# Kernel tuning notes

Hardware: AMD Instinct MI355X
Metric: run time of the kernel (lower is better)

The kernel has to match this reference:

```python
import jax, jax.numpy as jnp
import numpy as np
import math

D_MODEL = 1024
NUM_HEADS = 16
N_GROUP = 4
HEAD_DIM = D_MODEL // NUM_HEADS  # 64
KV_DIM = N_GROUP * HEAD_DIM      # 256
BS, SEQ = 2, 2048


def setup_inputs() -> dict:
    key = jax.random.key(0)
    ks = jax.random.split(key, 7)
    s = 0.02
    return {
        "h": jax.random.normal(ks[0], (BS, SEQ, D_MODEL), dtype=jnp.float32),
        "wq_w": jax.random.normal(ks[1], (D_MODEL, D_MODEL), dtype=jnp.float32) * s,
        "wq_b": jnp.zeros((D_MODEL,), dtype=jnp.float32),
        "wk_w": jax.random.normal(ks[2], (KV_DIM, D_MODEL), dtype=jnp.float32) * s,
        "wk_b": jnp.zeros((KV_DIM,), dtype=jnp.float32),
        "wv_w": jax.random.normal(ks[3], (KV_DIM, D_MODEL), dtype=jnp.float32) * s,
        "wv_b": jnp.zeros((KV_DIM,), dtype=jnp.float32),
    }


def reference(h, wq_w, wq_b, wk_w, wk_b, wv_w, wv_b):
    bs, seq, _ = h.shape
    rep = NUM_HEADS // N_GROUP  # heads per KV group

    # Linear projections (torch Linear: x @ W.T + b)
    q = h @ wq_w.T + wq_b                     # [bs, seq, d_model]
    k = h @ wk_w.T + wk_b                     # [bs, seq, kv_dim]
    v = h @ wv_w.T + wv_b                     # [bs, seq, kv_dim]

    q = q.reshape(bs, seq, NUM_HEADS, HEAD_DIM).transpose(0, 2, 1, 3)  # [b,H,s,d]
    k = k.reshape(bs, seq, N_GROUP, HEAD_DIM)                          # [b,s,G,d]
    v = v.reshape(bs, seq, N_GROUP, HEAD_DIM)
    # torch .repeat(1,1,1,rep).view(...,num_heads,head_dim) maps head h -> group h//rep,
    # identical to repeating each group `rep` times consecutively along the head axis.
    k = jnp.repeat(k, rep, axis=2).transpose(0, 2, 1, 3)               # [b,H,s,d]
    v = jnp.repeat(v, rep, axis=2).transpose(0, 2, 1, 3)               # [b,H,s,d]

    scores = jnp.einsum("bhqd,bhkd->bhqk", q, k) / math.sqrt(HEAD_DIM)
    attn = jax.nn.softmax(scores, axis=-1)
    out = jnp.einsum("bhqk,bhkd->bhqd", attn, v)                       # [b,H,s,d]
    out = out.transpose(0, 2, 1, 3).reshape(bs, seq, NUM_HEADS * HEAD_DIM)
    return out
```

## Files before the change

kernel.cpp:

```cpp
#include <hip/hip_runtime.h>

typedef _Float16 f16;
typedef _Float16 f16x8 __attribute__((ext_vector_type(8)));
typedef _Float16 f16x4 __attribute__((ext_vector_type(4)));
typedef float f32x4 __attribute__((ext_vector_type(4)));

#define MFMA16(a, b, c) __builtin_amdgcn_mfma_f32_16x16x32_f16((a), (b), (c), 0, 0, 0)
#define GLDS16(g, l)                                                        \
    __builtin_amdgcn_global_load_lds(                                       \
        (const __attribute__((address_space(1))) void*)(g),                 \
        (__attribute__((address_space(3))) void*)(l), 16, 0, 0)

#define SEQ 2048
#define DMODEL 1024
#define NH 16
#define NG 4

__global__ __launch_bounds__(256) void cvt_f16(const float* __restrict__ src,
                                               f16* __restrict__ dst, int n4) {
    int i = blockIdx.x * 256 + threadIdx.x;
    if (i < n4) {
        const float4 v = ((const float4*)src)[i];
        f16x4 p;
        p[0] = (f16)v.x; p[1] = (f16)v.y; p[2] = (f16)v.z; p[3] = (f16)v.w;
        ((f16x4*)dst)[i] = p;
    }
}

__global__ __launch_bounds__(256) void qkv_gemm(const f16* __restrict__ hA,
                                                const f16* __restrict__ wq,
                                                const f16* __restrict__ wk,
                                                const f16* __restrict__ wv,
                                                const float* __restrict__ bq,
                                                const float* __restrict__ bk,
                                                const float* __restrict__ bv,
                                                f16* __restrict__ Qb,
                                                f16* __restrict__ Kb,
                                                f16* __restrict__ Vtb,
                                                float qscale) {
    __shared__ __align__(16) f16 As[128 * 32];
    __shared__ __align__(16) f16 Bs[128 * 32];

    const int tid  = threadIdx.x;
    const int lane = tid & 63;
    const int l15  = lane & 15;
    const int l4   = lane >> 4;
    const int wave = tid >> 6;
    const int wm   = (wave >> 1) * 64;
    const int wn   = (wave & 1) * 64;
    const int bx   = blockIdx.x;
    const int m0   = blockIdx.y * 128;

    const f16* Bmat; const float* bias; f16* C; int N, n0; float osc; int vmode;
    if (bx < 8)       { Bmat = wq; bias = bq; C = Qb;  N = 1024; n0 = bx * 128;        osc = qscale; vmode = 0; }
    else if (bx < 10) { Bmat = wk; bias = bk; C = Kb;  N = 256;  n0 = (bx - 8) * 128;  osc = 1.0f;   vmode = 0; }
    else              { Bmat = wv; bias = bv; C = Vtb; N = 256;  n0 = (bx - 10) * 128; osc = 1.0f;   vmode = 1; }

    const int rowA = tid >> 2;
    const int colA = (tid & 3) * 8;
    const f16* Ag = hA   + (size_t)(m0 + rowA) * DMODEL + colA;
    const f16* Bg = Bmat + (size_t)(n0 + rowA) * DMODEL + colA;
    f16* AsW0 = As + wave * 512;
    f16* AsW1 = As + 2048 + wave * 512;
    f16* BsW0 = Bs + wave * 512;
    f16* BsW1 = Bs + 2048 + wave * 512;

    f32x4 acc[4][4];
#pragma unroll
    for (int i = 0; i < 4; i++)
#pragma unroll
        for (int j = 0; j < 4; j++) acc[i][j] = (f32x4)0.0f;

    for (int k0 = 0; k0 < DMODEL; k0 += 32) {
        GLDS16(Ag + k0,         AsW0);
        GLDS16(Ag + 65536 + k0, AsW1);
        GLDS16(Bg + k0,         BsW0);
        GLDS16(Bg + 65536 + k0, BsW1);
        __syncthreads();

        f16x8 af[4], bf[4];
#pragma unroll
        for (int i = 0; i < 4; i++)
            af[i] = *(const f16x8*)&As[(wm + i * 16 + l15) * 32 + l4 * 8];
#pragma unroll
        for (int j = 0; j < 4; j++)
            bf[j] = *(const f16x8*)&Bs[(wn + j * 16 + l15) * 32 + l4 * 8];
#pragma unroll
        for (int i = 0; i < 4; i++)
#pragma unroll
            for (int j = 0; j < 4; j++)
                acc[i][j] = MFMA16(af[i], bf[j], acc[i][j]);
        __syncthreads();
    }

#pragma unroll
    for (int i = 0; i < 4; i++) {
        const int mbase = m0 + wm + i * 16 + l4 * 4;
#pragma unroll
        for (int j = 0; j < 4; j++) {
            const int n  = n0 + wn + j * 16 + l15;
            const float bv = bias[n];
            if (vmode == 0) {
#pragma unroll
                for (int r = 0; r < 4; r++)
                    C[(size_t)(mbase + r) * N + n] = (f16)((acc[i][j][r] + bv) * osc);
            } else {
                f16x4 p;
#pragma unroll
                for (int r = 0; r < 4; r++)
                    p[r] = (f16)((acc[i][j][r] + bv) * osc);
                const int bb = mbase >> 11;
                const int s  = mbase & 2047;
                *(f16x4*)&C[((size_t)(bb * 256 + n)) * SEQ + s] = p;
            }
        }
    }
}

__global__ __launch_bounds__(256, 4) void attn_kernel(const f16* __restrict__ Q,
                                                      const f16* __restrict__ Kt,
                                                      const f16* __restrict__ Vt,
                                                      float* __restrict__ out) {
    __shared__ __align__(16) f16 Ks[64 * 72];
    __shared__ __align__(16) f16 Vs[64 * 72];
    __shared__ __align__(16) f16 Ps[64 * 72];

    const int tid  = threadIdx.x;
    const int lane = tid & 63;
    const int l15  = lane & 15;
    const int l4   = lane >> 4;
    const int wave = tid >> 6;
    const int b    = blockIdx.z;
    const int hh   = blockIdx.y;
    const int g    = hh >> 2;
    const int q0   = blockIdx.x * 64;
    const int qw   = wave * 16;

    f16x8 qf[2];
#pragma unroll
    for (int kt = 0; kt < 2; kt++)
        qf[kt] = *(const f16x8*)&Q[((size_t)(b * SEQ + q0 + qw + l15)) * DMODEL + hh * 64 + kt * 32 + l4 * 8];

    f32x4 oacc[4];
    float lsum[4];
#pragma unroll
    for (int dt = 0; dt < 4; dt++) oacc[dt] = (f32x4)0.0f;
#pragma unroll
    for (int r = 0; r < 4; r++) lsum[r] = 0.0f;

    const int srow = tid >> 2;
    const int sc8  = (tid & 3) * 8;
    const f16* Kg = Kt + (size_t)(b * SEQ + srow) * 256 + g * 64 + sc8;
    const f16* Vg = Vt + (size_t)(b * 256 + g * 64 + srow) * SEQ + sc8;

    for (int kb = 0; kb < SEQ; kb += 64) {
        *(f16x8*)&Ks[srow * 72 + sc8]      = *(const f16x8*)(Kg + (size_t)kb * 256);
        *(f16x8*)&Ks[srow * 72 + 32 + sc8] = *(const f16x8*)(Kg + (size_t)kb * 256 + 32);
        *(f16x8*)&Vs[srow * 72 + sc8]      = *(const f16x8*)(Vg + kb);
        *(f16x8*)&Vs[srow * 72 + 32 + sc8] = *(const f16x8*)(Vg + kb + 32);
        __syncthreads();

        f32x4 sacc[4];
#pragma unroll
        for (int jt = 0; jt < 4; jt++) sacc[jt] = (f32x4)0.0f;
#pragma unroll
        for (int jt = 0; jt < 4; jt++) {
            const f16x8 kf0 = *(const f16x8*)&Ks[(jt * 16 + l15) * 72 + l4 * 8];
            const f16x8 kf1 = *(const f16x8*)&Ks[(jt * 16 + l15) * 72 + 32 + l4 * 8];
            sacc[jt] = MFMA16(qf[0], kf0, sacc[jt]);
            sacc[jt] = MFMA16(qf[1], kf1, sacc[jt]);
        }

#pragma unroll
        for (int jt = 0; jt < 4; jt++)
#pragma unroll
            for (int r = 0; r < 4; r++) {
                const float p = exp2f(fminf(sacc[jt][r], 14.0f));
                lsum[r] += p;
                Ps[(qw + l4 * 4 + r) * 72 + jt * 16 + l15] = (f16)p;
            }

#pragma unroll
        for (int kt = 0; kt < 2; kt++) {
            const f16x8 pf = *(const f16x8*)&Ps[(qw + l15) * 72 + kt * 32 + l4 * 8];
#pragma unroll
            for (int dt = 0; dt < 4; dt++) {
                const f16x8 vf = *(const f16x8*)&Vs[(dt * 16 + l15) * 72 + kt * 32 + l4 * 8];
                oacc[dt] = MFMA16(pf, vf, oacc[dt]);
            }
        }
        __syncthreads();
    }

#pragma unroll
    for (int r = 0; r < 4; r++) {
        float l = lsum[r];
        l += __shfl_xor(l, 1);
        l += __shfl_xor(l, 2);
        l += __shfl_xor(l, 4);
        l += __shfl_xor(l, 8);
        const float inv = 1.0f / l;
        const int q = q0 + qw + l4 * 4 + r;
        float* op = out + ((size_t)(b * SEQ + q)) * DMODEL + hh * 64;
#pragma unroll
        for (int dt = 0; dt < 4; dt++)
            op[dt * 16 + l15] = oacc[dt][r] * inv;
    }
}

extern "C" void kernel_launch(void* const* d_in, const int* in_sizes, int n_in,
                              void* d_out, int out_size, void* d_ws, size_t ws_size,
                              hipStream_t stream) {
    const float* h    = (const float*)d_in[0];
    const float* wq_w = (const float*)d_in[1];
    const float* wq_b = (const float*)d_in[2];
    const float* wk_w = (const float*)d_in[3];
    const float* wk_b = (const float*)d_in[4];
    const float* wv_w = (const float*)d_in[5];
    const float* wv_b = (const float*)d_in[6];
    float* out = (float*)d_out;

    char* ws = (char*)d_ws;
    f16* hb  = (f16*)(ws + 0);
    f16* wqb = (f16*)(ws + 8388608);
    f16* wkb = (f16*)(ws + 10485760);
    f16* wvb = (f16*)(ws + 11010048);
    f16* Qb  = (f16*)(ws + 11534336);
    f16* Kb  = (f16*)(ws + 19922944);
    f16* Vtb = (f16*)(ws + 22020096);

    cvt_f16<<<4096, 256, 0, stream>>>(h, hb, 1048576);
    cvt_f16<<<1024, 256, 0, stream>>>(wq_w, wqb, 262144);
    cvt_f16<<<256,  256, 0, stream>>>(wk_w, wkb, 65536);
    cvt_f16<<<256,  256, 0, stream>>>(wv_w, wvb, 65536);

    const float qscale = 0.125f * 1.4426950408889634f;
    qkv_gemm<<<dim3(12, 32), 256, 0, stream>>>(hb, wqb, wkb, wvb, wq_b, wk_b, wv_b,
                                               Qb, Kb, Vtb, qscale);

    attn_kernel<<<dim3(32, 16, 2), 256, 0, stream>>>(Qb, Kb, Vtb, out);
}
```

Baseline: 191.0 us.

## Fuse conversions, narrow GEMM tiles, process two heads per attention block

The four fp32-to-fp16 conversion launches become one kernel. The QKV GEMM N-tile shrinks from 128 to 64, doubling the grid to 768 blocks for better CU fill. The attention kernel now handles two heads of the same KV group per block, so each staged K/V tile is reused twice and K/V global loads are halved. LDS padding changes to 76. The cost is more registers and LDS per attention block (occupancy hint lowered to 2) and only 512 attention blocks.

Result: no change. 191.6 us (+0.3%).

```diff
diff --git a/kernel.cpp b/kernel.cpp
--- a/kernel.cpp
+++ b/kernel.cpp
@@ -15,31 +15,39 @@
 #define DMODEL 1024
 #define NH 16
 #define NG 4
-
-__global__ __launch_bounds__(256) void cvt_f16(const float* __restrict__ src,
-                                               f16* __restrict__ dst, int n4) {
-    int i = blockIdx.x * 256 + threadIdx.x;
-    if (i < n4) {
-        const float4 v = ((const float4*)src)[i];
-        f16x4 p;
-        p[0] = (f16)v.x; p[1] = (f16)v.y; p[2] = (f16)v.z; p[3] = (f16)v.w;
-        ((f16x4*)dst)[i] = p;
-    }
-}
-
-__global__ __launch_bounds__(256) void qkv_gemm(const f16* __restrict__ hA,
-                                                const f16* __restrict__ wq,
-                                                const f16* __restrict__ wk,
-                                                const f16* __restrict__ wv,
-                                                const float* __restrict__ bq,
-                                                const float* __restrict__ bk,
-                                                const float* __restrict__ bv,
-                                                f16* __restrict__ Qb,
-                                                f16* __restrict__ Kb,
-                                                f16* __restrict__ Vtb,
-                                                float qscale) {
+#define PAD 76
+
+__global__ __launch_bounds__(256) void cvt_all(const float* __restrict__ h,
+                                               const float* __restrict__ wq,
+                                               const float* __restrict__ wk,
+                                               const float* __restrict__ wv,
+                                               f16* __restrict__ hb, f16* __restrict__ wqb,
+                                               f16* __restrict__ wkb, f16* __restrict__ wvb) {
+    const int i = blockIdx.x * 256 + threadIdx.x;
+    const float* s; f16* d; int off;
+    if (i < 1048576)      { s = h;  d = hb;  off = i; }
+    else if (i < 1310720) { s = wq; d = wqb; off = i - 1048576; }
+    else if (i < 1376256) { s = wk; d = wkb; off = i - 1310720; }
+    else                  { s = wv; d = wvb; off = i - 1376256; }
+    const float4 v = ((const float4*)s)[off];
+    f16x4 p;
+    p[0] = (f16)v.x; p[1] = (f16)v.y; p[2] = (f16)v.z; p[3] = (f16)v.w;
+    ((f16x4*)d)[off] = p;
+}
+
+__global__ __launch_bounds__(256, 3) void qkv_gemm(const f16* __restrict__ hA,
+                                                   const f16* __restrict__ wq,
+                                                   const f16* __restrict__ wk,
+                                                   const f16* __restrict__ wv,
+                                                   const float* __restrict__ bq,
+                                                   const float* __restrict__ bk,
+                                                   const float* __restrict__ bv,
+                                                   f16* __restrict__ Qb,
+                                                   f16* __restrict__ Kb,
+                                                   f16* __restrict__ Vtb,
+                                                   float qscale) {
     __shared__ __align__(16) f16 As[128 * 32];
-    __shared__ __align__(16) f16 Bs[128 * 32];
+    __shared__ __align__(16) f16 Bs[64 * 32];
 
     const int tid  = threadIdx.x;
     const int lane = tid & 63;
@@ -47,48 +55,46 @@
     const int l4   = lane >> 4;
     const int wave = tid >> 6;
     const int wm   = (wave >> 1) * 64;
-    const int wn   = (wave & 1) * 64;
+    const int wn   = (wave & 1) * 32;
     const int bx   = blockIdx.x;
     const int m0   = blockIdx.y * 128;
 
-    const f16* Bmat; const float* bias; f16* C; int N, n0; float osc; int vmode;
-    if (bx < 8)       { Bmat = wq; bias = bq; C = Qb;  N = 1024; n0 = bx * 128;        osc = qscale; vmode = 0; }
-    else if (bx < 10) { Bmat = wk; bias = bk; C = Kb;  N = 256;  n0 = (bx - 8) * 128;  osc = 1.0f;   vmode = 0; }
-    else              { Bmat = wv; bias = bv; C = Vtb; N = 256;  n0 = (bx - 10) * 128; osc = 1.0f;   vmode = 1; }
-
-    const int rowA = tid >> 2;
-    const int colA = (tid & 3) * 8;
-    const f16* Ag = hA   + (size_t)(m0 + rowA) * DMODEL + colA;
-    const f16* Bg = Bmat + (size_t)(n0 + rowA) * DMODEL + colA;
+    const f16* W; const float* bias; f16* C; int N, n0; float osc; int vmode;
+    if (bx < 16)      { W = wq; bias = bq; C = Qb;  N = 1024; n0 = bx * 64;        osc = qscale; vmode = 0; }
+    else if (bx < 20) { W = wk; bias = bk; C = Kb;  N = 256;  n0 = (bx - 16) * 64; osc = 1.0f;   vmode = 0; }
+    else              { W = wv; bias = bv; C = Vtb; N = 256;  n0 = (bx - 20) * 64; osc = 1.0f;   vmode = 1; }
+
+    const int rowT = tid >> 2;
+    const int colT = (tid & 3) * 8;
+    const f16* Ag = hA + (size_t)(m0 + rowT) * DMODEL + colT;
+    const f16* Bg = W  + (size_t)(n0 + rowT) * DMODEL + colT;
     f16* AsW0 = As + wave * 512;
     f16* AsW1 = As + 2048 + wave * 512;
-    f16* BsW0 = Bs + wave * 512;
-    f16* BsW1 = Bs + 2048 + wave * 512;
-
-    f32x4 acc[4][4];
+    f16* BsW  = Bs + wave * 512;
+
+    f32x4 acc[4][2];
 #pragma unroll
     for (int i = 0; i < 4; i++)
 #pragma unroll
-        for (int j = 0; j < 4; j++) acc[i][j] = (f32x4)0.0f;
+        for (int j = 0; j < 2; j++) acc[i][j] = (f32x4)0.0f;
 
     for (int k0 = 0; k0 < DMODEL; k0 += 32) {
         GLDS16(Ag + k0,         AsW0);
         GLDS16(Ag + 65536 + k0, AsW1);
-        GLDS16(Bg + k0,         BsW0);
-        GLDS16(Bg + 65536 + k0, BsW1);
-        __syncthreads();
-
-        f16x8 af[4], bf[4];
+        GLDS16(Bg + k0,         BsW);
+        __syncthreads();
+
+        f16x8 af[4], bf[2];
 #pragma unroll
         for (int i = 0; i < 4; i++)
             af[i] = *(const f16x8*)&As[(wm + i * 16 + l15) * 32 + l4 * 8];
 #pragma unroll
-        for (int j = 0; j < 4; j++)
+        for (int j = 0; j < 2; j++)
             bf[j] = *(const f16x8*)&Bs[(wn + j * 16 + l15) * 32 + l4 * 8];
 #pragma unroll
         for (int i = 0; i < 4; i++)
 #pragma unroll
-            for (int j = 0; j < 4; j++)
+            for (int j = 0; j < 2; j++)
                 acc[i][j] = MFMA16(af[i], bf[j], acc[i][j]);
         __syncthreads();
     }
@@ -97,7 +103,7 @@
     for (int i = 0; i < 4; i++) {
         const int mbase = m0 + wm + i * 16 + l4 * 4;
 #pragma unroll
-        for (int j = 0; j < 4; j++) {
+        for (int j = 0; j < 2; j++) {
             const int n  = n0 + wn + j * 16 + l15;
             const float bv = bias[n];
             if (vmode == 0) {
@@ -117,13 +123,13 @@
     }
 }
 
-__global__ __launch_bounds__(256, 4) void attn_kernel(const f16* __restrict__ Q,
+__global__ __launch_bounds__(256, 2) void attn_kernel(const f16* __restrict__ Q,
                                                       const f16* __restrict__ Kt,
                                                       const f16* __restrict__ Vt,
                                                       float* __restrict__ out) {
-    __shared__ __align__(16) f16 Ks[64 * 72];
-    __shared__ __align__(16) f16 Vs[64 * 72];
-    __shared__ __align__(16) f16 Ps[64 * 72];
+    __shared__ __align__(16) f16 Ks[64 * PAD];
+    __shared__ __align__(16) f16 Vs[64 * PAD];
+    __shared__ __align__(16) f16 Ps[128 * PAD];
 
     const int tid  = threadIdx.x;
     const int lane = tid & 63;
@@ -131,22 +137,29 @@
     const int l4   = lane >> 4;
     const int wave = tid >> 6;
     const int b    = blockIdx.z;
-    const int hh   = blockIdx.y;
-    const int g    = hh >> 2;
+    const int hp   = blockIdx.y;
+    const int g    = hp >> 1;
     const int q0   = blockIdx.x * 64;
     const int qw   = wave * 16;
 
-    f16x8 qf[2];
-#pragma unroll
-    for (int kt = 0; kt < 2; kt++)
-        qf[kt] = *(const f16x8*)&Q[((size_t)(b * SEQ + q0 + qw + l15)) * DMODEL + hh * 64 + kt * 32 + l4 * 8];
-
-    f32x4 oacc[4];
-    float lsum[4];
-#pragma unroll
-    for (int dt = 0; dt < 4; dt++) oacc[dt] = (f32x4)0.0f;
-#pragma unroll
-    for (int r = 0; r < 4; r++) lsum[r] = 0.0f;
+    f16x8 qf[2][2];
+#pragma unroll
+    for (int h = 0; h < 2; h++)
+#pragma unroll
+        for (int kt = 0; kt < 2; kt++)
+            qf[h][kt] = *(const f16x8*)&Q[((size_t)(b * SEQ + q0 + qw + l15)) * DMODEL
+                                          + (hp * 2 + h) * 64 + kt * 32 + l4 * 8];
+
+    f32x4 oacc[2][4];
+    float lsum[2][4];
+#pragma unroll
+    for (int h = 0; h < 2; h++)
+#pragma unroll
+        for (int dt = 0; dt < 4; dt++) oacc[h][dt] = (f32x4)0.0f;
+#pragma unroll
+    for (int h = 0; h < 2; h++)
+#pragma unroll
+        for (int r = 0; r < 4; r++) lsum[h][r] = 0.0f;
 
     const int srow = tid >> 2;
     const int sc8  = (tid & 3) * 8;
@@ -154,58 +167,69 @@
     const f16* Vg = Vt + (size_t)(b * 256 + g * 64 + srow) * SEQ + sc8;
 
     for (int kb = 0; kb < SEQ; kb += 64) {
-        *(f16x8*)&Ks[srow * 72 + sc8]      = *(const f16x8*)(Kg + (size_t)kb * 256);
-        *(f16x8*)&Ks[srow * 72 + 32 + sc8] = *(const f16x8*)(Kg + (size_t)kb * 256 + 32);
-        *(f16x8*)&Vs[srow * 72 + sc8]      = *(const f16x8*)(Vg + kb);
-        *(f16x8*)&Vs[srow * 72 + 32 + sc8] = *(const f16x8*)(Vg + kb + 32);
-        __syncthreads();
-
-        f32x4 sacc[4];
-#pragma unroll
-        for (int jt = 0; jt < 4; jt++) sacc[jt] = (f32x4)0.0f;
+        *(f16x8*)&Ks[srow * PAD + sc8]      = *(const f16x8*)(Kg + (size_t)kb * 256);
+        *(f16x8*)&Ks[srow * PAD + 32 + sc8] = *(const f16x8*)(Kg + (size_t)kb * 256 + 32);
+        *(f16x8*)&Vs[srow * PAD + sc8]      = *(const f16x8*)(Vg + kb);
+        *(f16x8*)&Vs[srow * PAD + 32 + sc8] = *(const f16x8*)(Vg + kb + 32);
+        __syncthreads();
+
+        f32x4 sacc[2][4];
+#pragma unroll
+        for (int h = 0; h < 2; h++)
+#pragma unroll
+            for (int jt = 0; jt < 4; jt++) sacc[h][jt] = (f32x4)0.0f;
 #pragma unroll
         for (int jt = 0; jt < 4; jt++) {
-            const f16x8 kf0 = *(const f16x8*)&Ks[(jt * 16 + l15) * 72 + l4 * 8];
-            const f16x8 kf1 = *(const f16x8*)&Ks[(jt * 16 + l15) * 72 + 32 + l4 * 8];
-            sacc[jt] = MFMA16(qf[0], kf0, sacc[jt]);
-            sacc[jt] = MFMA16(qf[1], kf1, sacc[jt]);
-        }
-
-#pragma unroll
-        for (int jt = 0; jt < 4; jt++)
-#pragma unroll
-            for (int r = 0; r < 4; r++) {
-                const float p = exp2f(fminf(sacc[jt][r], 14.0f));
-                lsum[r] += p;
-                Ps[(qw + l4 * 4 + r) * 72 + jt * 16 + l15] = (f16)p;
+            const f16x8 kf0 = *(const f16x8*)&Ks[(jt * 16 + l15) * PAD + l4 * 8];
+            const f16x8 kf1 = *(const f16x8*)&Ks[(jt * 16 + l15) * PAD + 32 + l4 * 8];
+#pragma unroll
+            for (int h = 0; h < 2; h++) {
+                sacc[h][jt] = MFMA16(qf[h][0], kf0, sacc[h][jt]);
+                sacc[h][jt] = MFMA16(qf[h][1], kf1, sacc[h][jt]);
             }
+        }
+
+#pragma unroll
+        for (int h = 0; h < 2; h++)
+#pragma unroll
+            for (int jt = 0; jt < 4; jt++)
+#pragma unroll
+                for (int r = 0; r < 4; r++) {
+                    const float p = exp2f(fminf(sacc[h][jt][r], 14.0f));
+                    lsum[h][r] += p;
+                    Ps[(h * 64 + qw + l4 * 4 + r) * PAD + jt * 16 + l15] = (f16)p;
+                }
 
 #pragma unroll
         for (int kt = 0; kt < 2; kt++) {
-            const f16x8 pf = *(const f16x8*)&Ps[(qw + l15) * 72 + kt * 32 + l4 * 8];
+            const f16x8 pf0 = *(const f16x8*)&Ps[(qw + l15) * PAD + kt * 32 + l4 * 8];
+            const f16x8 pf1 = *(const f16x8*)&Ps[(64 + qw + l15) * PAD + kt * 32 + l4 * 8];
 #pragma unroll
             for (int dt = 0; dt < 4; dt++) {
-                const f16x8 vf = *(const f16x8*)&Vs[(dt * 16 + l15) * 72 + kt * 32 + l4 * 8];
-                oacc[dt] = MFMA16(pf, vf, oacc[dt]);
+                const f16x8 vf = *(const f16x8*)&Vs[(dt * 16 + l15) * PAD + kt * 32 + l4 * 8];
+                oacc[0][dt] = MFMA16(pf0, vf, oacc[0][dt]);
+                oacc[1][dt] = MFMA16(pf1, vf, oacc[1][dt]);
             }
         }
         __syncthreads();
     }
 
 #pragma unroll
-    for (int r = 0; r < 4; r++) {
-        float l = lsum[r];
-        l += __shfl_xor(l, 1);
-        l += __shfl_xor(l, 2);
-        l += __shfl_xor(l, 4);
-        l += __shfl_xor(l, 8);
-        const float inv = 1.0f / l;
-        const int q = q0 + qw + l4 * 4 + r;
-        float* op = out + ((size_t)(b * SEQ + q)) * DMODEL + hh * 64;
-#pragma unroll
-        for (int dt = 0; dt < 4; dt++)
-            op[dt * 16 + l15] = oacc[dt][r] * inv;
-    }
+    for (int h = 0; h < 2; h++)
+#pragma unroll
+        for (int r = 0; r < 4; r++) {
+            float l = lsum[h][r];
+            l += __shfl_xor(l, 1);
+            l += __shfl_xor(l, 2);
+            l += __shfl_xor(l, 4);
+            l += __shfl_xor(l, 8);
+            const float inv = 1.0f / l;
+            const int q = q0 + qw + l4 * 4 + r;
+            float* op = out + ((size_t)(b * SEQ + q)) * DMODEL + (hp * 2 + h) * 64;
+#pragma unroll
+            for (int dt = 0; dt < 4; dt++)
+                op[dt * 16 + l15] = oacc[h][dt][r] * inv;
+        }
 }
 
 extern "C" void kernel_launch(void* const* d_in, const int* in_sizes, int n_in,
@@ -229,14 +253,11 @@
     f16* Kb  = (f16*)(ws + 19922944);
     f16* Vtb = (f16*)(ws + 22020096);
 
-    cvt_f16<<<4096, 256, 0, stream>>>(h, hb, 1048576);
-    cvt_f16<<<1024, 256, 0, stream>>>(wq_w, wqb, 262144);
-    cvt_f16<<<256,  256, 0, stream>>>(wk_w, wkb, 65536);
-    cvt_f16<<<256,  256, 0, stream>>>(wv_w, wvb, 65536);
+    cvt_all<<<5632, 256, 0, stream>>>(h, wq_w, wk_w, wv_w, hb, wqb, wkb, wvb);
 
     const float qscale = 0.125f * 1.4426950408889634f;
-    qkv_gemm<<<dim3(12, 32), 256, 0, stream>>>(hb, wqb, wkb, wvb, wq_b, wk_b, wv_b,
+    qkv_gemm<<<dim3(24, 32), 256, 0, stream>>>(hb, wqb, wkb, wvb, wq_b, wk_b, wv_b,
                                                Qb, Kb, Vtb, qscale);
 
-    attn_kernel<<<dim3(32, 16, 2), 256, 0, stream>>>(Qb, Kb, Vtb, out);
-}
+    attn_kernel<<<dim3(32, 8, 2), 256, 0, stream>>>(Qb, Kb, Vtb, out);
+}
```
